# Performance work log

Measured on AMD Instinct MI355X. Metric: run time of the kernel, lower is better.

The kernel has to match this reference:

```python
import jax, jax.numpy as jnp
import numpy as np

TEMPERATURE = 8.0  # sqrt(head_dim=64)


def setup_inputs() -> dict:
    key = jax.random.key(0)
    kq, kk, kv, km = jax.random.split(key, 4)
    B, S, D = 16, 2048, 64
    q = jax.random.normal(kq, (B, S, D), dtype=jnp.float32)
    k = jax.random.normal(kk, (B, S, D), dtype=jnp.float32)
    v = jax.random.normal(kv, (B, S, D), dtype=jnp.float32)
    mask = jax.random.randint(km, (B, S, S), 0, 2).astype(jnp.bool_)
    return {"q": q, "k": k, "v": v, "mask": mask}


def reference(q, k, v, mask):
    # latent = q @ k^T / temperature  -> [B, Sq, Sk]
    latent = jnp.einsum('bqd,bkd->bqk', q, k) / TEMPERATURE
    # NOTE: the original fills masked positions with 1e-9 (NOT -inf); keep faithful.
    latent = jnp.where(mask, jnp.float32(1e-9), latent)
    attn = jax.nn.softmax(latent, axis=-1)
    return jnp.einsum('bqk,bkd->bqd', attn, v)
```

## Files before the change

### kernel.cpp

```cpp
#include <hip/hip_runtime.h>
#include <hip/hip_bf16.h>

#define BB 16
#define SS 2048
#define DD 64
#define NT (SS / 64)
#define BUFS 20992

typedef __attribute__((ext_vector_type(8)))  unsigned short ushort8;
typedef __attribute__((ext_vector_type(8)))  __bf16 bf16x8;
typedef __attribute__((ext_vector_type(16))) float f32x16;

static __device__ __forceinline__ unsigned short f2bf(float x) {
    return __builtin_bit_cast(unsigned short, __float2bfloat16(x));
}
static __device__ __forceinline__ unsigned pk2f(float a, float b) {
    return (unsigned)f2bf(a) | ((unsigned)f2bf(b) << 16);
}
union F4 { float4 v; float a[4]; };

__global__ __launch_bounds__(256, 2)
void sdpa_mfma_kernel(const float* __restrict__ Q, const float* __restrict__ K,
                      const float* __restrict__ V, const unsigned int* __restrict__ M,
                      float* __restrict__ O) {
    __shared__ __align__(16) char smem[8192 + 2 * BUFS];
    char* Qs = smem;

    const int t    = threadIdx.x;
    const int lane = t & 63;
    const int l31  = lane & 31;
    const int half = lane >> 5;
    const int w    = t >> 6;
    const int qs   = w & 1;
    const int kh   = w >> 1;
    const int b    = blockIdx.y;
    const int q0   = blockIdx.x * 64;

    const float* Qg = Q + ((size_t)b * SS + q0) * DD;
    const float* Kg = K + (size_t)b * SS * DD;
    const float* Vg = V + (size_t)b * SS * DD;
    const unsigned int* Mg = M + (size_t)b * SS * SS + (size_t)q0 * SS;

    const int sr  = t >> 2;
    const int scm = t & 3;
    const int d0v = (t & 15) * 4;
    const int kkv = (t >> 4) * 4;
    const int kr0 = t >> 3;
    const int kg0 = t & 7;

    F4 ka0, ka1, ka2, ka3, va0, va1, va2, va3;
    uint4 ma0, ma1, ma2, ma3;

#define LOAD_TILE(KT) do {                                                     \
        const float* kp_ = Kg + (size_t)(KT) * 64 * DD + 8 * t;                \
        ka0.v = *(const float4*)(kp_);                                         \
        ka1.v = *(const float4*)(kp_ + 4);                                     \
        ka2.v = *(const float4*)(kp_ + 2048);                                  \
        ka3.v = *(const float4*)(kp_ + 2052);                                  \
        const float* vp_ = Vg + (size_t)((KT) * 64 + kkv) * DD + d0v;          \
        va0.v = *(const float4*)(vp_);                                         \
        va1.v = *(const float4*)(vp_ + DD);                                    \
        va2.v = *(const float4*)(vp_ + 2 * DD);                                \
        va3.v = *(const float4*)(vp_ + 3 * DD);                                \
        const unsigned int* mp_ = Mg + (size_t)sr * SS + (KT) * 64 + scm * 16; \
        ma0 = *(const uint4*)(mp_);                                            \
        ma1 = *(const uint4*)(mp_ + 4);                                        \
        ma2 = *(const uint4*)(mp_ + 8);                                        \
        ma3 = *(const uint4*)(mp_ + 12);                                       \
    } while (0)

#define WRITE_TILE(Kp, Vp, Mp) do {                                            \
        ushort8 u_;                                                            \
        _Pragma("unroll")                                                      \
        for (int e = 0; e < 4; e++) { u_[e] = f2bf(ka0.a[e]); u_[e+4] = f2bf(ka1.a[e]); } \
        *(ushort8*)((Kp) + kr0 * 128 + ((kg0 ^ (kr0 & 7)) * 16)) = u_;         \
        _Pragma("unroll")                                                      \
        for (int e = 0; e < 4; e++) { u_[e] = f2bf(ka2.a[e]); u_[e+4] = f2bf(ka3.a[e]); } \
        *(ushort8*)((Kp) + (kr0 + 32) * 128 + ((kg0 ^ (kr0 & 7)) * 16)) = u_;  \
        _Pragma("unroll")                                                      \
        for (int e = 0; e < 4; e++) {                                          \
            const int d_ = d0v + e;                                            \
            *(uint2*)((Vp) + d_ * 128 + (((kkv >> 3) ^ (d_ & 7)) * 16) + (kkv & 7) * 2) \
                = make_uint2(pk2f(va0.a[e], va1.a[e]), pk2f(va2.a[e], va3.a[e])); \
        }                                                                      \
        const unsigned w0_ = (ma0.x?1u:0u)|(ma0.y?0x100u:0u)|(ma0.z?0x10000u:0u)|(ma0.w?0x1000000u:0u); \
        const unsigned w1_ = (ma1.x?1u:0u)|(ma1.y?0x100u:0u)|(ma1.z?0x10000u:0u)|(ma1.w?0x1000000u:0u); \
        const unsigned w2_ = (ma2.x?1u:0u)|(ma2.y?0x100u:0u)|(ma2.z?0x10000u:0u)|(ma2.w?0x1000000u:0u); \
        const unsigned w3_ = (ma3.x?1u:0u)|(ma3.y?0x100u:0u)|(ma3.z?0x10000u:0u)|(ma3.w?0x1000000u:0u); \
        *(uint2*)((Mp) + sr * 72 + scm * 16)     = make_uint2(w0_, w1_);       \
        *(uint2*)((Mp) + sr * 72 + scm * 16 + 8) = make_uint2(w2_, w3_);       \
    } while (0)

    LOAD_TILE(0);

    {
        F4 f0, f1, f2, f3;
        const float* src = Qg + sr * DD + scm * 16;
        f0.v = *(const float4*)(src);
        f1.v = *(const float4*)(src + 4);
        f2.v = *(const float4*)(src + 8);
        f3.v = *(const float4*)(src + 12);
        ushort8 u0, u1;
        #pragma unroll
        for (int e = 0; e < 4; e++) {
            u0[e]     = f2bf(f0.a[e] * 0.125f);
            u0[e + 4] = f2bf(f1.a[e] * 0.125f);
            u1[e]     = f2bf(f2.a[e] * 0.125f);
            u1[e + 4] = f2bf(f3.a[e] * 0.125f);
        }
        *(ushort8*)(Qs + sr * 128 + (((scm * 2)     ^ (sr & 7)) * 16)) = u0;
        *(ushort8*)(Qs + sr * 128 + (((scm * 2 + 1) ^ (sr & 7)) * 16)) = u1;
    }
    __syncthreads();

    const int qrow = 32 * qs + l31;
    ushort8 bq[4];
    #pragma unroll
    for (int dc = 0; dc < 4; dc++)
        bq[dc] = *(const ushort8*)(Qs + qrow * 128 + (((2 * dc + half) ^ (qrow & 7)) * 16));

    f32x16 On0, On1;
    #pragma unroll
    for (int i = 0; i < 16; i++) { On0[i] = 0.f; On1[i] = 0.f; }
    float den_acc = 0.f;

    const int krow = 32 * kh + l31;

    for (int kt = 0; kt < NT; ++kt) {
        char* base = smem + 8192 + (kt & 1) * BUFS;
        char* Kp = base;
        char* Vp = base + 8192;
        char* Mp = base + 16384;

        WRITE_TILE(Kp, Vp, Mp);
        if (kt + 1 < NT) LOAD_TILE(kt + 1);
        __syncthreads();

        f32x16 S;
        #pragma unroll
        for (int i = 0; i < 16; i++) S[i] = 0.f;
        #pragma unroll
        for (int dc = 0; dc < 4; dc++) {
            bf16x8 ak = __builtin_bit_cast(bf16x8,
                *(const ushort8*)(Kp + krow * 128 + (((2 * dc + half) ^ (krow & 7)) * 16)));
            S = __builtin_amdgcn_mfma_f32_32x32x16_bf16(
                    ak, __builtin_bit_cast(bf16x8, bq[dc]), S, 0, 0, 0);
        }

        float p[16];
        #pragma unroll
        for (int g = 0; g < 4; g++) {
            const unsigned mw = *(const unsigned*)(Mp + qrow * 72 + 32 * kh + 8 * g + 4 * half);
            #pragma unroll
            for (int e = 0; e < 4; e++) {
                const float ev = __expf(S[4 * g + e]);
                const float pv = ((mw >> (8 * e)) & 0xffu) ? 1.0f : ev;
                p[4 * g + e] = pv;
                den_acc += pv;
            }
        }

        #pragma unroll
        for (int s2 = 0; s2 < 2; s2++) {
            const unsigned o0 = pk2f(p[8 * s2 + 0], p[8 * s2 + 1]);
            const unsigned o1 = pk2f(p[8 * s2 + 2], p[8 * s2 + 3]);
            const unsigned o2 = pk2f(p[8 * s2 + 4], p[8 * s2 + 5]);
            const unsigned o3 = pk2f(p[8 * s2 + 6], p[8 * s2 + 7]);
            const unsigned s0 = half ? o0 : o2;
            const unsigned s1 = half ? o1 : o3;
            const unsigned r0 = (unsigned)__shfl_xor((int)s0, 32, 64);
            const unsigned r1 = (unsigned)__shfl_xor((int)s1, 32, 64);
            uint4 bu;
            bu.x = half ? r0 : o0;
            bu.y = half ? r1 : o1;
            bu.z = half ? o2 : r0;
            bu.w = half ? o3 : r1;
            const bf16x8 bp = __builtin_bit_cast(bf16x8, bu);
            #pragma unroll
            for (int dc = 0; dc < 2; dc++) {
                const int vrow = 32 * dc + l31;
                bf16x8 av = __builtin_bit_cast(bf16x8,
                    *(const ushort8*)(Vp + vrow * 128 +
                        (((4 * kh + 2 * s2 + half) ^ (vrow & 7)) * 16)));
                if (dc == 0) On0 = __builtin_amdgcn_mfma_f32_32x32x16_bf16(av, bp, On0, 0, 0, 0);
                else         On1 = __builtin_amdgcn_mfma_f32_32x32x16_bf16(av, bp, On1, 0, 0, 0);
            }
        }
    }

    const float den_tot = den_acc + __shfl_xor(den_acc, 32, 64);
    float* red  = (float*)smem;
    float* denx = (float*)(smem + 16384);

    __syncthreads();
    if (kh == 1) {
        #pragma unroll
        for (int dc = 0; dc < 2; dc++)
            #pragma unroll
            for (int g = 0; g < 4; g++) {
                const f32x16& Oc = dc ? On1 : On0;
                float4 st;
                st.x = Oc[4 * g + 0]; st.y = Oc[4 * g + 1];
                st.z = Oc[4 * g + 2]; st.w = Oc[4 * g + 3];
                *(float4*)((char*)red + qs * 8192 + (dc * 4 + g) * 1024 + lane * 16) = st;
            }
        if (lane < 32) denx[qs * 32 + l31] = den_tot;
    }
    __syncthreads();
    if (kh == 0) {
        const float inv = 1.0f / (den_tot + denx[qs * 32 + l31]);
        float* Og = O + ((size_t)b * SS + q0 + qrow) * DD;
        #pragma unroll
        for (int dc = 0; dc < 2; dc++)
            #pragma unroll
            for (int g = 0; g < 4; g++) {
                const float4 pr = *(const float4*)((char*)red + qs * 8192 + (dc * 4 + g) * 1024 + lane * 16);
                const f32x16& Oc = dc ? On1 : On0;
                float4 st;
                st.x = (Oc[4 * g + 0] + pr.x) * inv;
                st.y = (Oc[4 * g + 1] + pr.y) * inv;
                st.z = (Oc[4 * g + 2] + pr.z) * inv;
                st.w = (Oc[4 * g + 3] + pr.w) * inv;
                *(float4*)(Og + 32 * dc + 8 * g + 4 * half) = st;
            }
    }
#undef LOAD_TILE
#undef WRITE_TILE
}

extern "C" void kernel_launch(void* const* d_in, const int* in_sizes, int n_in,
                              void* d_out, int out_size, void* d_ws, size_t ws_size,
                              hipStream_t stream) {
    const float* q = (const float*)d_in[0];
    const float* k = (const float*)d_in[1];
    const float* v = (const float*)d_in[2];
    const unsigned int* m = (const unsigned int*)d_in[3];
    float* out = (float*)d_out;

    dim3 grid(SS / 64, BB);
    sdpa_mfma_kernel<<<grid, 256, 0, stream>>>(q, k, v, m, out);
}
```

Before: 394.5 us.

## Load K and mask per-wave into registers, drop block barriers in main loop

Each wave now loads its own K rows and mask entries straight from global memory into the register layout the MFMA operands need, so the shared K and mask staging tiles and the per-iteration __syncthreads go away. V is transposed through a small private per-wave LDS slice. Mask and K/V loads for the next tile are software-pipelined in registers with a two-way unrolled ping-pong. The aim is to remove block-wide barriers and shared-memory round trips. In exchange, K and V are loaded redundantly by the waves that share them, register pressure rises, and the private V slice is written and read with no wave-level fence.

```diff
diff --git a/kernel.cpp b/kernel.cpp
--- a/kernel.cpp
+++ b/kernel.cpp
@@ -5,7 +5,6 @@
 #define SS 2048
 #define DD 64
 #define NT (SS / 64)
-#define BUFS 20992
 
 typedef __attribute__((ext_vector_type(8)))  unsigned short ushort8;
 typedef __attribute__((ext_vector_type(8)))  __bf16 bf16x8;
@@ -23,7 +22,7 @@
 void sdpa_mfma_kernel(const float* __restrict__ Q, const float* __restrict__ K,
                       const float* __restrict__ V, const unsigned int* __restrict__ M,
                       float* __restrict__ O) {
-    __shared__ __align__(16) char smem[8192 + 2 * BUFS];
+    __shared__ __align__(16) char smem[8192 + 4 * 5120];
     char* Qs = smem;
 
     const int t    = threadIdx.x;
@@ -35,65 +34,34 @@
     const int kh   = w >> 1;
     const int b    = blockIdx.y;
     const int q0   = blockIdx.x * 64;
+    char* Vw = smem + 8192 + w * 5120;
 
     const float* Qg = Q + ((size_t)b * SS + q0) * DD;
     const float* Kg = K + (size_t)b * SS * DD;
     const float* Vg = V + (size_t)b * SS * DD;
     const unsigned int* Mg = M + (size_t)b * SS * SS + (size_t)q0 * SS;
 
-    const int sr  = t >> 2;
-    const int scm = t & 3;
-    const int d0v = (t & 15) * 4;
-    const int kkv = (t >> 4) * 4;
-    const int kr0 = t >> 3;
-    const int kg0 = t & 7;
-
-    F4 ka0, ka1, ka2, ka3, va0, va1, va2, va3;
-    uint4 ma0, ma1, ma2, ma3;
-
-#define LOAD_TILE(KT) do {                                                     \
-        const float* kp_ = Kg + (size_t)(KT) * 64 * DD + 8 * t;                \
-        ka0.v = *(const float4*)(kp_);                                         \
-        ka1.v = *(const float4*)(kp_ + 4);                                     \
-        ka2.v = *(const float4*)(kp_ + 2048);                                  \
-        ka3.v = *(const float4*)(kp_ + 2052);                                  \
-        const float* vp_ = Vg + (size_t)((KT) * 64 + kkv) * DD + d0v;          \
-        va0.v = *(const float4*)(vp_);                                         \
-        va1.v = *(const float4*)(vp_ + DD);                                    \
-        va2.v = *(const float4*)(vp_ + 2 * DD);                                \
-        va3.v = *(const float4*)(vp_ + 3 * DD);                                \
-        const unsigned int* mp_ = Mg + (size_t)sr * SS + (KT) * 64 + scm * 16; \
-        ma0 = *(const uint4*)(mp_);                                            \
-        ma1 = *(const uint4*)(mp_ + 4);                                        \
-        ma2 = *(const uint4*)(mp_ + 8);                                        \
-        ma3 = *(const uint4*)(mp_ + 12);                                       \
-    } while (0)
-
-#define WRITE_TILE(Kp, Vp, Mp) do {                                            \
-        ushort8 u_;                                                            \
-        _Pragma("unroll")                                                      \
-        for (int e = 0; e < 4; e++) { u_[e] = f2bf(ka0.a[e]); u_[e+4] = f2bf(ka1.a[e]); } \
-        *(ushort8*)((Kp) + kr0 * 128 + ((kg0 ^ (kr0 & 7)) * 16)) = u_;         \
-        _Pragma("unroll")                                                      \
-        for (int e = 0; e < 4; e++) { u_[e] = f2bf(ka2.a[e]); u_[e+4] = f2bf(ka3.a[e]); } \
-        *(ushort8*)((Kp) + (kr0 + 32) * 128 + ((kg0 ^ (kr0 & 7)) * 16)) = u_;  \
-        _Pragma("unroll")                                                      \
-        for (int e = 0; e < 4; e++) {                                          \
-            const int d_ = d0v + e;                                            \
-            *(uint2*)((Vp) + d_ * 128 + (((kkv >> 3) ^ (d_ & 7)) * 16) + (kkv & 7) * 2) \
-                = make_uint2(pk2f(va0.a[e], va1.a[e]), pk2f(va2.a[e], va3.a[e])); \
-        }                                                                      \
-        const unsigned w0_ = (ma0.x?1u:0u)|(ma0.y?0x100u:0u)|(ma0.z?0x10000u:0u)|(ma0.w?0x1000000u:0u); \
-        const unsigned w1_ = (ma1.x?1u:0u)|(ma1.y?0x100u:0u)|(ma1.z?0x10000u:0u)|(ma1.w?0x1000000u:0u); \
-        const unsigned w2_ = (ma2.x?1u:0u)|(ma2.y?0x100u:0u)|(ma2.z?0x10000u:0u)|(ma2.w?0x1000000u:0u); \
-        const unsigned w3_ = (ma3.x?1u:0u)|(ma3.y?0x100u:0u)|(ma3.z?0x10000u:0u)|(ma3.w?0x1000000u:0u); \
-        *(uint2*)((Mp) + sr * 72 + scm * 16)     = make_uint2(w0_, w1_);       \
-        *(uint2*)((Mp) + sr * 72 + scm * 16 + 8) = make_uint2(w2_, w3_);       \
-    } while (0)
-
-    LOAD_TILE(0);
+    const int gk  = lane >> 4;
+    const int d0v = (lane & 15) * 4;
+    const float* kp = Kg + (size_t)(32 * kh + l31) * DD + 8 * half;
+    const float* vp = Vg + (size_t)(32 * kh + 8 * gk) * DD + d0v;
+    const unsigned int* mp = Mg + (size_t)(32 * qs + l31) * SS + 32 * kh + 4 * half;
+
+    F4 kf[8], vf[8];
+    uint4 mfA[4], mfB[4];
+
+    #pragma unroll
+    for (int dc = 0; dc < 4; dc++) {
+        kf[2 * dc].v     = *(const float4*)(kp + 16 * dc);
+        kf[2 * dc + 1].v = *(const float4*)(kp + 16 * dc + 4);
+    }
+    #pragma unroll
+    for (int r = 0; r < 8; r++) vf[r].v = *(const float4*)(vp + r * DD);
+    #pragma unroll
+    for (int g = 0; g < 4; g++) mfA[g] = *(const uint4*)(mp + 8 * g);
 
     {
+        const int sr = t >> 2, scm = t & 3;
         F4 f0, f1, f2, f3;
         const float* src = Qg + sr * DD + scm * 16;
         f0.v = *(const float4*)(src);
@@ -114,79 +82,113 @@
     __syncthreads();
 
     const int qrow = 32 * qs + l31;
-    ushort8 bq[4];
+    bf16x8 bq[4];
     #pragma unroll
     for (int dc = 0; dc < 4; dc++)
-        bq[dc] = *(const ushort8*)(Qs + qrow * 128 + (((2 * dc + half) ^ (qrow & 7)) * 16));
+        bq[dc] = __builtin_bit_cast(bf16x8, *(const ushort8*)(
+            Qs + qrow * 128 + (((2 * dc + half) ^ (qrow & 7)) * 16)));
 
     f32x16 On0, On1;
     #pragma unroll
     for (int i = 0; i < 16; i++) { On0[i] = 0.f; On1[i] = 0.f; }
     float den_acc = 0.f;
 
-    const int krow = 32 * kh + l31;
-
-    for (int kt = 0; kt < NT; ++kt) {
-        char* base = smem + 8192 + (kt & 1) * BUFS;
-        char* Kp = base;
-        char* Vp = base + 8192;
-        char* Mp = base + 16384;
-
-        WRITE_TILE(Kp, Vp, Mp);
-        if (kt + 1 < NT) LOAD_TILE(kt + 1);
-        __syncthreads();
-
-        f32x16 S;
-        #pragma unroll
-        for (int i = 0; i < 16; i++) S[i] = 0.f;
-        #pragma unroll
-        for (int dc = 0; dc < 4; dc++) {
-            bf16x8 ak = __builtin_bit_cast(bf16x8,
-                *(const ushort8*)(Kp + krow * 128 + (((2 * dc + half) ^ (krow & 7)) * 16)));
-            S = __builtin_amdgcn_mfma_f32_32x32x16_bf16(
-                    ak, __builtin_bit_cast(bf16x8, bq[dc]), S, 0, 0, 0);
-        }
-
-        float p[16];
-        #pragma unroll
-        for (int g = 0; g < 4; g++) {
-            const unsigned mw = *(const unsigned*)(Mp + qrow * 72 + 32 * kh + 8 * g + 4 * half);
-            #pragma unroll
-            for (int e = 0; e < 4; e++) {
-                const float ev = __expf(S[4 * g + e]);
-                const float pv = ((mw >> (8 * e)) & 0xffu) ? 1.0f : ev;
-                p[4 * g + e] = pv;
-                den_acc += pv;
-            }
-        }
-
-        #pragma unroll
-        for (int s2 = 0; s2 < 2; s2++) {
-            const unsigned o0 = pk2f(p[8 * s2 + 0], p[8 * s2 + 1]);
-            const unsigned o1 = pk2f(p[8 * s2 + 2], p[8 * s2 + 3]);
-            const unsigned o2 = pk2f(p[8 * s2 + 4], p[8 * s2 + 5]);
-            const unsigned o3 = pk2f(p[8 * s2 + 6], p[8 * s2 + 7]);
-            const unsigned s0 = half ? o0 : o2;
-            const unsigned s1 = half ? o1 : o3;
-            const unsigned r0 = (unsigned)__shfl_xor((int)s0, 32, 64);
-            const unsigned r1 = (unsigned)__shfl_xor((int)s1, 32, 64);
-            uint4 bu;
-            bu.x = half ? r0 : o0;
-            bu.y = half ? r1 : o1;
-            bu.z = half ? o2 : r0;
-            bu.w = half ? o3 : r1;
-            const bf16x8 bp = __builtin_bit_cast(bf16x8, bu);
-            #pragma unroll
-            for (int dc = 0; dc < 2; dc++) {
-                const int vrow = 32 * dc + l31;
-                bf16x8 av = __builtin_bit_cast(bf16x8,
-                    *(const ushort8*)(Vp + vrow * 128 +
-                        (((4 * kh + 2 * s2 + half) ^ (vrow & 7)) * 16)));
-                if (dc == 0) On0 = __builtin_amdgcn_mfma_f32_32x32x16_bf16(av, bp, On0, 0, 0, 0);
-                else         On1 = __builtin_amdgcn_mfma_f32_32x32x16_bf16(av, bp, On1, 0, 0, 0);
-            }
-        }
-    }
+#define ITER(MC, MN, KT) do {                                                  \
+    const int ktn_ = ((KT) + 1 < NT) ? (KT) + 1 : NT - 1;                      \
+            \
+    {                                                                          \
+        const unsigned int* mpp_ = mp + (size_t)ktn_ * 64;                     \
+        _Pragma("unroll")                                                      \
+        for (int g = 0; g < 4; g++) MN[g] = *(const uint4*)(mpp_ + 8 * g);     \
+    }                                                                          \
+                                   \
+    bf16x8 ak_[4];                                                             \
+    _Pragma("unroll")                                                          \
+    for (int dc = 0; dc < 4; dc++) {                                           \
+        ushort8 u_;                                                            \
+        _Pragma("unroll")                                                      \
+        for (int e = 0; e < 4; e++) {                                          \
+            u_[e]     = f2bf(kf[2 * dc].a[e]);                                 \
+            u_[e + 4] = f2bf(kf[2 * dc + 1].a[e]);                             \
+        }                                                                      \
+        ak_[dc] = __builtin_bit_cast(bf16x8, u_);                              \
+    }                                                                          \
+                                            \
+    f32x16 S_;                                                                 \
+    _Pragma("unroll")                                                          \
+    for (int i = 0; i < 16; i++) S_[i] = 0.f;                                  \
+    _Pragma("unroll")                                                          \
+    for (int dc = 0; dc < 4; dc++)                                             \
+        S_ = __builtin_amdgcn_mfma_f32_32x32x16_bf16(ak_[dc], bq[dc], S_, 0, 0, 0); \
+                             \
+    float p_[16];                                                              \
+    _Pragma("unroll")                                                          \
+    for (int g = 0; g < 4; g++) {                                              \
+        const unsigned mw_[4] = {MC[g].x, MC[g].y, MC[g].z, MC[g].w};          \
+        _Pragma("unroll")                                                      \
+        for (int e = 0; e < 4; e++) {                                          \
+            const float ev_ = __expf(S_[4 * g + e]);                           \
+            const float pv_ = mw_[e] ? 1.0f : ev_;                             \
+            p_[4 * g + e] = pv_;                                               \
+            den_acc += pv_;                                                    \
+        }                                                                      \
+    }                                                                          \
+        \
+    _Pragma("unroll")                                                          \
+    for (int e = 0; e < 4; e++) {                                              \
+        const int d_ = d0v + e;                                                \
+        uint4 pkv_;                                                            \
+        pkv_.x = pk2f(vf[0].a[e], vf[1].a[e]);                                 \
+        pkv_.y = pk2f(vf[2].a[e], vf[3].a[e]);                                 \
+        pkv_.z = pk2f(vf[4].a[e], vf[5].a[e]);                                 \
+        pkv_.w = pk2f(vf[6].a[e], vf[7].a[e]);                                 \
+        *(uint4*)(Vw + d_ * 80 + (((gk ^ (d_ >> 2)) & 3) * 16)) = pkv_;        \
+    }                                                                          \
+                               \
+    {                                                                          \
+        const float* kpp_ = kp + (size_t)ktn_ * 4096;                          \
+        _Pragma("unroll")                                                      \
+        for (int dc = 0; dc < 4; dc++) {                                       \
+            kf[2 * dc].v     = *(const float4*)(kpp_ + 16 * dc);               \
+            kf[2 * dc + 1].v = *(const float4*)(kpp_ + 16 * dc + 4);           \
+        }                                                                      \
+        const float* vpp_ = vp + (size_t)ktn_ * 4096;                          \
+        _Pragma("unroll")                                                      \
+        for (int r = 0; r < 8; r++) vf[r].v = *(const float4*)(vpp_ + r * DD); \
+    }                                                                          \
+                          \
+    _Pragma("unroll")                                                          \
+    for (int s2 = 0; s2 < 2; s2++) {                                           \
+        const unsigned o0 = pk2f(p_[8 * s2 + 0], p_[8 * s2 + 1]);              \
+        const unsigned o1 = pk2f(p_[8 * s2 + 2], p_[8 * s2 + 3]);              \
+        const unsigned o2 = pk2f(p_[8 * s2 + 4], p_[8 * s2 + 5]);              \
+        const unsigned o3 = pk2f(p_[8 * s2 + 6], p_[8 * s2 + 7]);              \
+        const unsigned s0 = half ? o0 : o2;                                    \
+        const unsigned s1 = half ? o1 : o3;                                    \
+        const unsigned r0 = (unsigned)__shfl_xor((int)s0, 32, 64);             \
+        const unsigned r1 = (unsigned)__shfl_xor((int)s1, 32, 64);             \
+        uint4 bu;                                                              \
+        bu.x = half ? r0 : o0;                                                 \
+        bu.y = half ? r1 : o1;                                                 \
+        bu.z = half ? o2 : r0;                                                 \
+        bu.w = half ? o3 : r1;                                                 \
+        const bf16x8 bp = __builtin_bit_cast(bf16x8, bu);                      \
+        _Pragma("unroll")                                                      \
+        for (int dc2 = 0; dc2 < 2; dc2++) {                                    \
+            const int vrow = 32 * dc2 + l31;                                   \
+            bf16x8 av = __builtin_bit_cast(bf16x8, *(const ushort8*)(          \
+                Vw + vrow * 80 + ((((2 * s2 + half) ^ (vrow >> 2)) & 3) * 16))); \
+            if (dc2 == 0) On0 = __builtin_amdgcn_mfma_f32_32x32x16_bf16(av, bp, On0, 0, 0, 0); \
+            else          On1 = __builtin_amdgcn_mfma_f32_32x32x16_bf16(av, bp, On1, 0, 0, 0); \
+        }                                                                      \
+    }                                                                          \
+} while (0)
+
+    for (int kt = 0; kt < NT; kt += 2) {
+        ITER(mfA, mfB, kt);
+        ITER(mfB, mfA, kt + 1);
+    }
+#undef ITER
 
     const float den_tot = den_acc + __shfl_xor(den_acc, 32, 64);
     float* red  = (float*)smem;
@@ -224,8 +226,6 @@
                 *(float4*)(Og + 32 * dc + 8 * g + 4 * half) = st;
             }
     }
-#undef LOAD_TILE
-#undef WRITE_TILE
 }
 
 extern "C" void kernel_launch(void* const* d_in, const int* in_sizes, int n_in,
```

Measured after the change: 437.4 us. 1.11x slower.
